# Kernel optimization log

Hardware: AMD Instinct MI355X
Metric: run time of the kernel (lower is better)

## Reference

```python
import jax, jax.numpy as jnp
import numpy as np

N_USERS = 100_000
N_ITEMS = 50_000
N_EDGES = 2_000_000
D = 64
ALPHA = 0.5      # tanh-blend coefficient (alpha)
NORM_2 = -1.0    # exponent on back-aggregation degree norm (args.norm_2)


def setup_inputs() -> dict:
    key = jax.random.key(0)
    k1, k2, k3, k4, k5 = jax.random.split(key, 5)
    return {
        "h_user": jax.random.normal(k1, (N_USERS, D), jnp.float32) * 0.1,
        "pretrained_feature": jax.random.normal(k2, (N_ITEMS, D), jnp.float32),
        "edge_w": jax.random.normal(k3, (N_ITEMS, 1), jnp.float32),
        "src_idx": jax.random.randint(k4, (N_EDGES,), 0, N_USERS, dtype=jnp.int32),
        "dst_idx": jax.random.randint(k5, (N_EDGES,), 0, N_ITEMS, dtype=jnp.int32),
    }


def reference(h_user, pretrained_feature, edge_w, src_idx, dst_idx):
    # HGCNLayer.forward: bidirectional copy_src+sum aggregation with degree norm,
    # tanh prompt blend and node-softmax edge weighting.
    ones = jnp.ones((N_EDGES,), h_user.dtype)

    # forward pass user -> item: rst[d] = sum_{(s,d) in E} h_user[s]
    rst = jax.ops.segment_sum(h_user[src_idx], dst_idx, num_segments=N_ITEMS)  # [N_ITEMS, D]
    deg_dst = jnp.clip(jax.ops.segment_sum(ones, dst_idx, num_segments=N_ITEMS), 1.0)

    # alpha * tanh prompt blend
    rst = rst + ALPHA * jnp.tanh(pretrained_feature)
    # edge-prompt softmax scaling (softmax over nodes; see notes)
    rst = jax.nn.softmax(edge_w, axis=0) * rst
    # in-degree^-1 normalization
    rst = rst / deg_dst[:, None]

    # backward pass item -> user: bsrc[s] = sum_{(s,d) in E} rst[d]
    bsrc = jax.ops.segment_sum(rst[dst_idx], src_idx, num_segments=N_USERS)  # [N_USERS, D]
    deg_src = jnp.clip(jax.ops.segment_sum(ones, src_idx, num_segments=N_USERS), 1.0)
    bsrc = bsrc * jnp.power(deg_src, NORM_2)[:, None]
    return bsrc
```

## Files before the change

### kernel.cpp

```cpp
#include <hip/hip_runtime.h>
#include <hip/hip_bf16.h>
#include <math.h>

#define N_USERS 100000
#define N_ITEMS 50000
#define N_EDGES 2000000
#define D 64

#define FB_BINS 98
#define BB_BINS 196
#define NBINS   (FB_BINS + BB_BINS)
#define CHUNK   2048
#define NCHUNK  ((N_EDGES + CHUNK - 1) / CHUNK)
#define NSH     4
#define FOFF_F_N (FB_BINS * 512 * NSH + 1)
#define FOFF_B_N (BB_BINS * 512 + 1)
#define TOTSLOT  (2 * N_EDGES)
#define PART_SLOTS (FB_BINS * 512 * NSH)
#define PASSA_WGS (((N_ITEMS + 31) / 32) * 8)
#define PASSB_WGS ((N_ITEMS + 7) / 8)
#define BWD_WGS ((N_USERS + 31) / 32)

__device__ __forceinline__ float blo(unsigned u) {
    union { unsigned i; float f; } c; c.i = u << 16; return c.f;
}
__device__ __forceinline__ float bhi(unsigned u) {
    union { unsigned i; float f; } c; c.i = u & 0xFFFF0000u; return c.f;
}
__device__ __forceinline__ unsigned bpack(float x, float y) {
    __hip_bfloat16 a = __float2bfloat16(x), b = __float2bfloat16(y);
    unsigned short ua = *reinterpret_cast<unsigned short*>(&a);
    unsigned short ub = *reinterpret_cast<unsigned short*>(&b);
    return (unsigned)ua | ((unsigned)ub << 16);
}

__global__ __launch_bounds__(256) void h2b_kernel(
    const float2* __restrict__ in, unsigned* __restrict__ out, int n) {
    int stride = gridDim.x * blockDim.x;
    for (int i = blockIdx.x * blockDim.x + threadIdx.x; i < n; i += stride) {
        float2 v = in[i];
        out[i] = bpack(v.x, v.y);
    }
}

__global__ __launch_bounds__(256) void hist_kernel(
    const int* __restrict__ src, const int* __restrict__ dst, int* __restrict__ gh) {
    __shared__ int h[NBINS];
    for (int i = threadIdx.x; i < NBINS; i += 256) h[i] = 0;
    __syncthreads();
    int stride = gridDim.x * blockDim.x;
    for (int e = blockIdx.x * blockDim.x + threadIdx.x; e < N_EDGES; e += stride) {
        atomicAdd(&h[dst[e] >> 9], 1);
        atomicAdd(&h[FB_BINS + (src[e] >> 9)], 1);
    }
    __syncthreads();
    for (int i = threadIdx.x; i < NBINS; i += 256) {
        int v = h[i];
        if (v) atomicAdd(&gh[i], v);
    }
}

__global__ void scan_excl(const int* __restrict__ in, int* __restrict__ out,
                          int* __restrict__ cur, int n) {
    const int T = 1024, E = 4;
    __shared__ int wsum[16];
    __shared__ int s_carry;
    if (threadIdx.x == 0) s_carry = 0;
    __syncthreads();

    int lane = threadIdx.x & 63;
    int wid  = threadIdx.x >> 6;

    for (int base = 0; base < n; base += T * E) {
        int idx0 = base + threadIdx.x * E;
        int v[E];
        int tot = 0;
#pragma unroll
        for (int e = 0; e < E; e++) {
            int i = idx0 + e;
            v[e] = (i < n) ? in[i] : 0;
            tot += v[e];
        }
        int incl = tot;
#pragma unroll
        for (int off = 1; off < 64; off <<= 1) {
            int t = __shfl_up(incl, off);
            if (lane >= off) incl += t;
        }
        if (lane == 63) wsum[wid] = incl;
        __syncthreads();
        if (wid == 0 && lane < 16) {
            int t = wsum[lane];
            int sc = t;
#pragma unroll
            for (int off = 1; off < 16; off <<= 1) {
                int u = __shfl_up(sc, off);
                if (lane >= off) sc += u;
            }
            wsum[lane] = sc - t;
        }
        __syncthreads();
        int wave_off = wsum[wid];
        int excl = s_carry + wave_off + incl - tot;
#pragma unroll
        for (int e = 0; e < E; e++) {
            int i = idx0 + e;
            if (i < n) { out[i] = excl; cur[i] = excl; }
            excl += v[e];
        }
        __syncthreads();
        if (threadIdx.x == T - 1) s_carry += wave_off + incl;
        __syncthreads();
    }
    if (threadIdx.x == 0) out[n] = s_carry;
}

__global__ __launch_bounds__(256) void binfill_kernel(
    const int* __restrict__ src, const int* __restrict__ dst,
    int* __restrict__ gcur, unsigned* __restrict__ stage) {
    __shared__ int cnt[NBINS];
    __shared__ int gbase[NBINS];
    __shared__ int lcur[NBINS];
    int c = blockIdx.x;
    int base = c * CHUNK;
    int nEdge = N_EDGES - base; if (nEdge > CHUNK) nEdge = CHUNK;

    for (int t = threadIdx.x; t < NBINS; t += 256) { cnt[t] = 0; lcur[t] = 0; }
    __syncthreads();

    int es[8], ed[8];
#pragma unroll
    for (int j = 0; j < 8; j++) {
        int k = j * 256 + threadIdx.x;
        if (k < nEdge) {
            es[j] = src[base + k];
            ed[j] = dst[base + k];
            atomicAdd(&cnt[ed[j] >> 9], 1);
            atomicAdd(&cnt[FB_BINS + (es[j] >> 9)], 1);
        } else {
            es[j] = -1;
        }
    }
    __syncthreads();
    for (int t = threadIdx.x; t < NBINS; t += 256) {
        int cv = cnt[t];
        gbase[t] = cv ? atomicAdd(&gcur[t], cv) : 0;
    }
    __syncthreads();
#pragma unroll
    for (int j = 0; j < 8; j++) {
        if (es[j] >= 0) {
            int s = es[j], d = ed[j];
            int bf = d >> 9;
            int p = atomicAdd(&lcur[bf], 1);
            stage[gbase[bf] + p] = (unsigned)s | ((unsigned)(d & 511) << 17);
            int bb = FB_BINS + (s >> 9);
            int q = atomicAdd(&lcur[bb], 1);
            stage[gbase[bb] + q] = (unsigned)d | ((unsigned)(s & 511) << 16);
        }
    }
}

__global__ __launch_bounds__(512) void redist3_kernel(
    const unsigned* __restrict__ stage, const int* __restrict__ binoff,
    unsigned* __restrict__ stage2, int* __restrict__ foff_f, int* __restrict__ foff_b) {
    __shared__ int cnt[512 * NSH];
    __shared__ int wsum[8];
    int wg = blockIdx.x, t = threadIdx.x, lane = t & 63, wv = t >> 6;

    if (wg < FB_BINS) {
        int B = wg;
        int beg = binoff[B], end = binoff[B + 1];
        for (int j = t; j < 512 * NSH; j += 512) cnt[j] = 0;
        __syncthreads();
        for (int k = beg + t; k < end; k += 512) {
            unsigned e = stage[k];
            atomicAdd(&cnt[(((e >> 17) & 511) << 2) | (e & 3)], 1);
        }
        __syncthreads();
        int c[NSH]; int tot = 0;
#pragma unroll
        for (int j = 0; j < NSH; j++) { c[j] = cnt[(t << 2) | j]; tot += c[j]; }
        int incl = tot;
#pragma unroll
        for (int off = 1; off < 64; off <<= 1) {
            int u = __shfl_up(incl, off);
            if (lane >= off) incl += u;
        }
        if (lane == 63) wsum[wv] = incl;
        __syncthreads();
        if (t == 0) {
            int run = 0;
#pragma unroll
            for (int k2 = 0; k2 < 8; k2++) { int x = wsum[k2]; wsum[k2] = run; run += x; }
        }
        __syncthreads();
        int base = beg + wsum[wv] + incl - tot;
        int slot0 = (((B << 9) | t) << 2);
#pragma unroll
        for (int j = 0; j < NSH; j++) {
            foff_f[slot0 + j] = base;
            cnt[(t << 2) | j] = base;
            base += c[j];
        }
        if (B == FB_BINS - 1 && t == 0) foff_f[FB_BINS * 512 * NSH] = end;
        __syncthreads();
        for (int k = beg + t; k < end; k += 512) {
            unsigned e = stage[k];
            int idx = (((e >> 17) & 511) << 2) | (e & 3);
            int p = atomicAdd(&cnt[idx], 1);
            stage2[p] = e & 0x1FFFFu;
        }
    } else {
        for (int pass = 0; pass < 2; pass++) {
            int B = FB_BINS + ((wg - FB_BINS) << 1) + pass;
            int beg = binoff[B], end = binoff[B + 1];
            cnt[t] = 0;
            __syncthreads();
            for (int k = beg + t; k < end; k += 512) {
                unsigned e = stage[k];
                atomicAdd(&cnt[(e >> 16) & 511], 1);
            }
            __syncthreads();
            int v = cnt[t];
            int incl = v;
#pragma unroll
            for (int off = 1; off < 64; off <<= 1) {
                int u = __shfl_up(incl, off);
                if (lane >= off) incl += u;
            }
            if (lane == 63) wsum[wv] = incl;
            __syncthreads();
            if (t == 0) {
                int run = 0;
#pragma unroll
                for (int k2 = 0; k2 < 8; k2++) { int x = wsum[k2]; wsum[k2] = run; run += x; }
            }
            __syncthreads();
            int base = beg + wsum[wv] + incl - v;
            foff_b[((B - FB_BINS) << 9) | t] = base;
            cnt[t] = base;
            if (B == NBINS - 1 && t == 0) foff_b[BB_BINS * 512] = end;
            __syncthreads();
            for (int k = beg + t; k < end; k += 512) {
                unsigned e = stage[k];
                int p = atomicAdd(&cnt[(e >> 16) & 511], 1);
                stage2[p] = e & 0xFFFFu;
            }
            __syncthreads();
        }
    }
}

__global__ void softmax_stats_kernel(const float* __restrict__ w, float* __restrict__ stats) {
    __shared__ float red[16];
    int tid = threadIdx.x, lane = tid & 63, wid = tid >> 6;

    float m = -INFINITY;
    for (int i = tid; i < N_ITEMS; i += 1024) m = fmaxf(m, w[i]);
#pragma unroll
    for (int off = 32; off; off >>= 1) m = fmaxf(m, __shfl_xor(m, off));
    if (lane == 0) red[wid] = m;
    __syncthreads();
    if (tid == 0) {
        float t = red[0];
        for (int k = 1; k < 16; k++) t = fmaxf(t, red[k]);
        red[0] = t;
    }
    __syncthreads();
    m = red[0];
    __syncthreads();

    float s = 0.f;
    for (int i = tid; i < N_ITEMS; i += 1024) s += expf(w[i] - m);
#pragma unroll
    for (int off = 32; off; off >>= 1) s += __shfl_xor(s, off);
    if (lane == 0) red[wid] = s;
    __syncthreads();
    if (tid == 0) {
        float t = 0.f;
        for (int k = 0; k < 16; k++) t += red[k];
        stats[0] = m;
        stats[1] = t;
    }
}

__global__ __launch_bounds__(256) void passA_fwd_kernel(
    const unsigned* __restrict__ hu16, const unsigned* __restrict__ stage2,
    const int* __restrict__ foff_f, unsigned* __restrict__ part) {
    int tid = threadIdx.x, lane = tid & 63, wv = tid >> 6;
    int q = lane & 31, half = lane >> 5;
    int ib = blockIdx.x >> 3, x = blockIdx.x & 7;
    int sh = x >> 1, hb = x & 1;
    int i0 = ib * 32 + hb * 16;

    for (int il = wv; il < 16; il += 4) {
        int i = i0 + il;
        if (i >= N_ITEMS) break;
        int slot = (i << 2) | sh;
        int a = foff_f[slot], b = foff_f[slot + 1];
        float ax = 0.f, ay = 0.f;
        int k = a;
        for (; k + 8 <= b; k += 8) {
            int s0 = (int)__builtin_nontemporal_load(&stage2[k + half]);
            int s1 = (int)__builtin_nontemporal_load(&stage2[k + 2 + half]);
            int s2 = (int)__builtin_nontemporal_load(&stage2[k + 4 + half]);
            int s3 = (int)__builtin_nontemporal_load(&stage2[k + 6 + half]);
            unsigned u0 = hu16[(s0 << 5) + q];
            unsigned u1 = hu16[(s1 << 5) + q];
            unsigned u2 = hu16[(s2 << 5) + q];
            unsigned u3 = hu16[(s3 << 5) + q];
            ax += (blo(u0) + blo(u1)) + (blo(u2) + blo(u3));
            ay += (bhi(u0) + bhi(u1)) + (bhi(u2) + bhi(u3));
        }
        for (; k + 2 <= b; k += 2) {
            unsigned u = hu16[((int)__builtin_nontemporal_load(&stage2[k + half]) << 5) + q];
            ax += blo(u); ay += bhi(u);
        }
        if (k < b && half == 0) {
            unsigned u = hu16[((int)__builtin_nontemporal_load(&stage2[k]) << 5) + q];
            ax += blo(u); ay += bhi(u);
        }
        ax += __shfl_xor(ax, 32);
        ay += __shfl_xor(ay, 32);
        if (half == 0)
            __builtin_nontemporal_store(bpack(ax, ay), &part[((size_t)slot << 5) + q]);
    }
}

__global__ __launch_bounds__(256) void passB_fwd_kernel(
    const unsigned* __restrict__ part, const float* __restrict__ pf,
    const float* __restrict__ edge_w, const int* __restrict__ foff_f,
    const float* __restrict__ stats, unsigned* __restrict__ rst16) {
    int tid = threadIdx.x, lane = tid & 63, wv = tid >> 6;
    int q = lane & 31, half = lane >> 5;
    int i = blockIdx.x * 8 + wv * 2 + half;
    if (i >= N_ITEMS) return;
    float m = stats[0], ssum = stats[1];
    float ax = 0.f, ay = 0.f;
#pragma unroll
    for (int s = 0; s < NSH; s++) {
        unsigned u = __builtin_nontemporal_load(&part[(((size_t)(i << 2) | s) << 5) + q]);
        ax += blo(u); ay += bhi(u);
    }
    int dg = foff_f[(i << 2) + 4] - foff_f[i << 2];
    float deg = dg < 1 ? 1.f : (float)dg;
    float sc = expf(edge_w[i] - m) / (ssum * deg);
    const float2* PF2 = (const float2*)pf;
    float2 pv = PF2[(size_t)i * 32 + q];
    float vx = (ax + 0.5f * tanhf(pv.x)) * sc;
    float vy = (ay + 0.5f * tanhf(pv.y)) * sc;
    rst16[(size_t)i * 32 + q] = bpack(vx, vy);
}

__global__ __launch_bounds__(256) void pass2_bwd_kernel(
    const unsigned* __restrict__ rst16, const unsigned* __restrict__ stage2,
    const int* __restrict__ foff_b, float* __restrict__ out) {
    int tid = threadIdx.x, lane = tid & 63, wv = tid >> 6;
    int q = lane & 31, half = lane >> 5;
    float2* OUT2 = (float2*)out;
    int u0i = blockIdx.x * 32;

    for (int il = wv; il < 32; il += 4) {
        int u = u0i + il;
        if (u >= N_USERS) break;
        int a = foff_b[u], b = foff_b[u + 1];
        float ax = 0.f, ay = 0.f;
        int k = a;
        for (; k + 8 <= b; k += 8) {
            int d0 = (int)__builtin_nontemporal_load(&stage2[k + half]);
            int d1 = (int)__builtin_nontemporal_load(&stage2[k + 2 + half]);
            int d2 = (int)__builtin_nontemporal_load(&stage2[k + 4 + half]);
            int d3 = (int)__builtin_nontemporal_load(&stage2[k + 6 + half]);
            unsigned u0 = rst16[(d0 << 5) + q];
            unsigned u1 = rst16[(d1 << 5) + q];
            unsigned u2 = rst16[(d2 << 5) + q];
            unsigned u3 = rst16[(d3 << 5) + q];
            ax += (blo(u0) + blo(u1)) + (blo(u2) + blo(u3));
            ay += (bhi(u0) + bhi(u1)) + (bhi(u2) + bhi(u3));
        }
        for (; k + 2 <= b; k += 2) {
            unsigned e = rst16[((int)__builtin_nontemporal_load(&stage2[k + half]) << 5) + q];
            ax += blo(e); ay += bhi(e);
        }
        if (k < b && half == 0) {
            unsigned e = rst16[((int)__builtin_nontemporal_load(&stage2[k]) << 5) + q];
            ax += blo(e); ay += bhi(e);
        }
        ax += __shfl_xor(ax, 32);
        ay += __shfl_xor(ay, 32);
        if (half == 0) {
            float deg = (float)(b - a);
            if (deg < 1.f) deg = 1.f;
            OUT2[(size_t)u * 32 + q] = make_float2(ax / deg, ay / deg);
        }
    }
}

extern "C" void kernel_launch(void* const* d_in, const int* in_sizes, int n_in,
                              void* d_out, int out_size, void* d_ws, size_t ws_size,
                              hipStream_t stream) {
    const float* h_user = (const float*)d_in[0];
    const float* pf     = (const float*)d_in[1];
    const float* edge_w = (const float*)d_in[2];
    const int*   src    = (const int*)d_in[3];
    const int*   dst    = (const int*)d_in[4];
    float* out = (float*)d_out;

    char* p = (char*)d_ws;
    int* gh      = (int*)p;     p += sizeof(int) * NBINS;
    int* binoff  = (int*)p;     p += sizeof(int) * (NBINS + 1);
    int* gcur    = (int*)p;     p += sizeof(int) * NBINS;
    int* foff_f  = (int*)p;     p += sizeof(int) * FOFF_F_N;
    int* foff_b  = (int*)p;     p += sizeof(int) * FOFF_B_N;
    float* stats = (float*)p;   p += 4 * sizeof(float);
    unsigned* part  = (unsigned*)p;
    unsigned* stage = part;
    p += sizeof(unsigned) * (size_t)PART_SLOTS * 32;
    unsigned* stage2 = (unsigned*)p; p += sizeof(unsigned) * (size_t)TOTSLOT;
    unsigned* hu16   = (unsigned*)p; p += sizeof(unsigned) * (size_t)N_USERS * 32;
    unsigned* rst16  = (unsigned*)p; p += sizeof(unsigned) * (size_t)N_ITEMS * 32;

    hipMemsetAsync(gh, 0, sizeof(int) * NBINS, stream);

    hist_kernel<<<256, 256, 0, stream>>>(src, dst, gh);
    scan_excl<<<1, 1024, 0, stream>>>(gh, binoff, gcur, NBINS);
    binfill_kernel<<<NCHUNK, 256, 0, stream>>>(src, dst, gcur, stage);
    redist3_kernel<<<196, 512, 0, stream>>>(stage, binoff, stage2, foff_f, foff_b);
    h2b_kernel<<<1024, 256, 0, stream>>>((const float2*)h_user, hu16, N_USERS * 32);
    softmax_stats_kernel<<<1, 1024, 0, stream>>>(edge_w, stats);
    passA_fwd_kernel<<<PASSA_WGS, 256, 0, stream>>>(hu16, stage2, foff_f, part);
    passB_fwd_kernel<<<PASSB_WGS, 256, 0, stream>>>(part, pf, edge_w, foff_f, stats, rst16);
    pass2_bwd_kernel<<<BWD_WGS, 256, 0, stream>>>(rst16, stage2, foff_b, out);
}
```

Measured before the change: 398.1 us.

## Fuse forward aggregation passes and merge prep kernels to cut launches

Drops the 4-way sharded forward partial-sum scheme (passA plus passB reduction through a part buffer) and replaces it with a single gather kernel per item that also applies the tanh blend, softmax scale and degree norm. The bf16 conversion of h_user is merged into the histogram kernel, and the softmax stats are merged into the scan kernel as a second block. The gather loops are unrolled to 16 edges and work-groups shrink to 16 nodes. This removes launches and the part-buffer round trip, but loses the parallelism the sharding gave to high-degree items.

Result: faster. 344.3 us (-13.5%).

```diff
diff --git a/kernel.cpp b/kernel.cpp
--- a/kernel.cpp
+++ b/kernel.cpp
@@ -12,14 +12,11 @@
 #define NBINS   (FB_BINS + BB_BINS)
 #define CHUNK   2048
 #define NCHUNK  ((N_EDGES + CHUNK - 1) / CHUNK)
-#define NSH     4
-#define FOFF_F_N (FB_BINS * 512 * NSH + 1)
+#define FOFF_F_N (FB_BINS * 512 + 1)
 #define FOFF_B_N (BB_BINS * 512 + 1)
 #define TOTSLOT  (2 * N_EDGES)
-#define PART_SLOTS (FB_BINS * 512 * NSH)
-#define PASSA_WGS (((N_ITEMS + 31) / 32) * 8)
-#define PASSB_WGS ((N_ITEMS + 7) / 8)
-#define BWD_WGS ((N_USERS + 31) / 32)
+#define FWD_WGS (N_ITEMS / 16)
+#define BWD_WGS ((N_USERS + 15) / 16)
 
 __device__ __forceinline__ float blo(unsigned u) {
     union { unsigned i; float f; } c; c.i = u << 16; return c.f;
@@ -34,22 +31,20 @@
     return (unsigned)ua | ((unsigned)ub << 16);
 }
 
-__global__ __launch_bounds__(256) void h2b_kernel(
-    const float2* __restrict__ in, unsigned* __restrict__ out, int n) {
-    int stride = gridDim.x * blockDim.x;
-    for (int i = blockIdx.x * blockDim.x + threadIdx.x; i < n; i += stride) {
-        float2 v = in[i];
-        out[i] = bpack(v.x, v.y);
-    }
-}
-
-__global__ __launch_bounds__(256) void hist_kernel(
-    const int* __restrict__ src, const int* __restrict__ dst, int* __restrict__ gh) {
+__global__ __launch_bounds__(256) void prep_kernel(
+    const float2* __restrict__ hin, unsigned* __restrict__ hu16,
+    const int* __restrict__ src, const int* __restrict__ dst,
+    int* __restrict__ gh) {
     __shared__ int h[NBINS];
     for (int i = threadIdx.x; i < NBINS; i += 256) h[i] = 0;
     __syncthreads();
     int stride = gridDim.x * blockDim.x;
-    for (int e = blockIdx.x * blockDim.x + threadIdx.x; e < N_EDGES; e += stride) {
+    int t0 = blockIdx.x * blockDim.x + threadIdx.x;
+    for (int i = t0; i < N_USERS * 32; i += stride) {
+        float2 v = hin[i];
+        hu16[i] = bpack(v.x, v.y);
+    }
+    for (int e = t0; e < N_EDGES; e += stride) {
         atomicAdd(&h[dst[e] >> 9], 1);
         atomicAdd(&h[FB_BINS + (src[e] >> 9)], 1);
     }
@@ -60,25 +55,20 @@
     }
 }
 
-__global__ void scan_excl(const int* __restrict__ in, int* __restrict__ out,
-                          int* __restrict__ cur, int n) {
-    const int T = 1024, E = 4;
+__global__ void scan_soft_kernel(const int* __restrict__ in, int* __restrict__ out,
+                                 int* __restrict__ cur,
+                                 const float* __restrict__ w, float* __restrict__ stats) {
+    __shared__ float redf[16];
     __shared__ int wsum[16];
-    __shared__ int s_carry;
-    if (threadIdx.x == 0) s_carry = 0;
-    __syncthreads();
-
-    int lane = threadIdx.x & 63;
-    int wid  = threadIdx.x >> 6;
-
-    for (int base = 0; base < n; base += T * E) {
-        int idx0 = base + threadIdx.x * E;
-        int v[E];
-        int tot = 0;
-#pragma unroll
-        for (int e = 0; e < E; e++) {
+    int tid = threadIdx.x, lane = tid & 63, wid = tid >> 6;
+
+    if (blockIdx.x == 0) {
+        int idx0 = tid * 4;
+        int v[4]; int tot = 0;
+#pragma unroll
+        for (int e = 0; e < 4; e++) {
             int i = idx0 + e;
-            v[e] = (i < n) ? in[i] : 0;
+            v[e] = (i < NBINS) ? in[i] : 0;
             tot += v[e];
         }
         int incl = tot;
@@ -100,19 +90,45 @@
             wsum[lane] = sc - t;
         }
         __syncthreads();
-        int wave_off = wsum[wid];
-        int excl = s_carry + wave_off + incl - tot;
-#pragma unroll
-        for (int e = 0; e < E; e++) {
+        int excl = wsum[wid] + incl - tot;
+#pragma unroll
+        for (int e = 0; e < 4; e++) {
             int i = idx0 + e;
-            if (i < n) { out[i] = excl; cur[i] = excl; }
+            if (i < NBINS) { out[i] = excl; cur[i] = excl; }
+            if (i == NBINS) out[i] = excl;
             excl += v[e];
         }
-        __syncthreads();
-        if (threadIdx.x == T - 1) s_carry += wave_off + incl;
-        __syncthreads();
-    }
-    if (threadIdx.x == 0) out[n] = s_carry;
+        if (tid == 1023) out[NBINS] = excl;
+        return;
+    }
+
+    float m = -INFINITY;
+    for (int i = tid; i < N_ITEMS; i += 1024) m = fmaxf(m, w[i]);
+#pragma unroll
+    for (int off = 32; off; off >>= 1) m = fmaxf(m, __shfl_xor(m, off));
+    if (lane == 0) redf[wid] = m;
+    __syncthreads();
+    if (tid == 0) {
+        float t = redf[0];
+        for (int k = 1; k < 16; k++) t = fmaxf(t, redf[k]);
+        redf[0] = t;
+    }
+    __syncthreads();
+    m = redf[0];
+    __syncthreads();
+
+    float s = 0.f;
+    for (int i = tid; i < N_ITEMS; i += 1024) s += expf(w[i] - m);
+#pragma unroll
+    for (int off = 32; off; off >>= 1) s += __shfl_xor(s, off);
+    if (lane == 0) redf[wid] = s;
+    __syncthreads();
+    if (tid == 0) {
+        float t = 0.f;
+        for (int k = 0; k < 16; k++) t += redf[k];
+        stats[0] = m;
+        stats[1] = t;
+    }
 }
 
 __global__ __launch_bounds__(256) void binfill_kernel(
@@ -164,24 +180,22 @@
 __global__ __launch_bounds__(512) void redist3_kernel(
     const unsigned* __restrict__ stage, const int* __restrict__ binoff,
     unsigned* __restrict__ stage2, int* __restrict__ foff_f, int* __restrict__ foff_b) {
-    __shared__ int cnt[512 * NSH];
+    __shared__ int cnt[512];
     __shared__ int wsum[8];
     int wg = blockIdx.x, t = threadIdx.x, lane = t & 63, wv = t >> 6;
 
     if (wg < FB_BINS) {
         int B = wg;
         int beg = binoff[B], end = binoff[B + 1];
-        for (int j = t; j < 512 * NSH; j += 512) cnt[j] = 0;
+        cnt[t] = 0;
         __syncthreads();
         for (int k = beg + t; k < end; k += 512) {
             unsigned e = stage[k];
-            atomicAdd(&cnt[(((e >> 17) & 511) << 2) | (e & 3)], 1);
-        }
-        __syncthreads();
-        int c[NSH]; int tot = 0;
-#pragma unroll
-        for (int j = 0; j < NSH; j++) { c[j] = cnt[(t << 2) | j]; tot += c[j]; }
-        int incl = tot;
+            atomicAdd(&cnt[(e >> 17) & 511], 1);
+        }
+        __syncthreads();
+        int v = cnt[t];
+        int incl = v;
 #pragma unroll
         for (int off = 1; off < 64; off <<= 1) {
             int u = __shfl_up(incl, off);
@@ -195,20 +209,14 @@
             for (int k2 = 0; k2 < 8; k2++) { int x = wsum[k2]; wsum[k2] = run; run += x; }
         }
         __syncthreads();
-        int base = beg + wsum[wv] + incl - tot;
-        int slot0 = (((B << 9) | t) << 2);
-#pragma unroll
-        for (int j = 0; j < NSH; j++) {
-            foff_f[slot0 + j] = base;
-            cnt[(t << 2) | j] = base;
-            base += c[j];
-        }
-        if (B == FB_BINS - 1 && t == 0) foff_f[FB_BINS * 512 * NSH] = end;
+        int base = beg + wsum[wv] + incl - v;
+        foff_f[(B << 9) | t] = base;
+        cnt[t] = base;
+        if (B == FB_BINS - 1 && t == 0) foff_f[FB_BINS * 512] = end;
         __syncthreads();
         for (int k = beg + t; k < end; k += 512) {
             unsigned e = stage[k];
-            int idx = (((e >> 17) & 511) << 2) | (e & 3);
-            int p = atomicAdd(&cnt[idx], 1);
+            int p = atomicAdd(&cnt[(e >> 17) & 511], 1);
             stage2[p] = e & 0x1FFFFu;
         }
     } else {
@@ -252,56 +260,46 @@
     }
 }
 
-__global__ void softmax_stats_kernel(const float* __restrict__ w, float* __restrict__ stats) {
-    __shared__ float red[16];
-    int tid = threadIdx.x, lane = tid & 63, wid = tid >> 6;
-
-    float m = -INFINITY;
-    for (int i = tid; i < N_ITEMS; i += 1024) m = fmaxf(m, w[i]);
-#pragma unroll
-    for (int off = 32; off; off >>= 1) m = fmaxf(m, __shfl_xor(m, off));
-    if (lane == 0) red[wid] = m;
-    __syncthreads();
-    if (tid == 0) {
-        float t = red[0];
-        for (int k = 1; k < 16; k++) t = fmaxf(t, red[k]);
-        red[0] = t;
-    }
-    __syncthreads();
-    m = red[0];
-    __syncthreads();
-
-    float s = 0.f;
-    for (int i = tid; i < N_ITEMS; i += 1024) s += expf(w[i] - m);
-#pragma unroll
-    for (int off = 32; off; off >>= 1) s += __shfl_xor(s, off);
-    if (lane == 0) red[wid] = s;
-    __syncthreads();
-    if (tid == 0) {
-        float t = 0.f;
-        for (int k = 0; k < 16; k++) t += red[k];
-        stats[0] = m;
-        stats[1] = t;
-    }
-}
-
-__global__ __launch_bounds__(256) void passA_fwd_kernel(
-    const unsigned* __restrict__ hu16, const unsigned* __restrict__ stage2,
-    const int* __restrict__ foff_f, unsigned* __restrict__ part) {
+__global__ __launch_bounds__(256) void fwd_gather_kernel(
+    const unsigned* __restrict__ hu16, const float* __restrict__ pf,
+    const float* __restrict__ edge_w, const unsigned* __restrict__ stage2,
+    const int* __restrict__ foff_f, const float* __restrict__ stats,
+    unsigned* __restrict__ rst16) {
     int tid = threadIdx.x, lane = tid & 63, wv = tid >> 6;
     int q = lane & 31, half = lane >> 5;
-    int ib = blockIdx.x >> 3, x = blockIdx.x & 7;
-    int sh = x >> 1, hb = x & 1;
-    int i0 = ib * 32 + hb * 16;
+    float m = stats[0], ssum = stats[1];
+    const float2* PF2 = (const float2*)pf;
+    int i0 = blockIdx.x * 16;
 
     for (int il = wv; il < 16; il += 4) {
         int i = i0 + il;
         if (i >= N_ITEMS) break;
-        int slot = (i << 2) | sh;
-        int a = foff_f[slot], b = foff_f[slot + 1];
+        int a = foff_f[i], b = foff_f[i + 1];
         float ax = 0.f, ay = 0.f;
         int k = a;
-        for (; k + 8 <= b; k += 8) {
+        for (; k + 16 <= b; k += 16) {
+            int s0 = (int)__builtin_nontemporal_load(&stage2[k + half]);
+            int s1 = (int)__builtin_nontemporal_load(&stage2[k + 2 + half]);
+            int s2 = (int)__builtin_nontemporal_load(&stage2[k + 4 + half]);
+            int s3 = (int)__builtin_nontemporal_load(&stage2[k + 6 + half]);
+            int s4 = (int)__builtin_nontemporal_load(&stage2[k + 8 + half]);
+            int s5 = (int)__builtin_nontemporal_load(&stage2[k + 10 + half]);
+            int s6 = (int)__builtin_nontemporal_load(&stage2[k + 12 + half]);
+            int s7 = (int)__builtin_nontemporal_load(&stage2[k + 14 + half]);
+            unsigned u0 = hu16[(s0 << 5) + q];
+            unsigned u1 = hu16[(s1 << 5) + q];
+            unsigned u2 = hu16[(s2 << 5) + q];
+            unsigned u3 = hu16[(s3 << 5) + q];
+            unsigned u4 = hu16[(s4 << 5) + q];
+            unsigned u5 = hu16[(s5 << 5) + q];
+            unsigned u6 = hu16[(s6 << 5) + q];
+            unsigned u7 = hu16[(s7 << 5) + q];
+            ax += ((blo(u0) + blo(u1)) + (blo(u2) + blo(u3)))
+                + ((blo(u4) + blo(u5)) + (blo(u6) + blo(u7)));
+            ay += ((bhi(u0) + bhi(u1)) + (bhi(u2) + bhi(u3)))
+                + ((bhi(u4) + bhi(u5)) + (bhi(u6) + bhi(u7)));
+        }
+        if (k + 8 <= b) {
             int s0 = (int)__builtin_nontemporal_load(&stage2[k + half]);
             int s1 = (int)__builtin_nontemporal_load(&stage2[k + 2 + half]);
             int s2 = (int)__builtin_nontemporal_load(&stage2[k + 4 + half]);
@@ -312,6 +310,7 @@
             unsigned u3 = hu16[(s3 << 5) + q];
             ax += (blo(u0) + blo(u1)) + (blo(u2) + blo(u3));
             ay += (bhi(u0) + bhi(u1)) + (bhi(u2) + bhi(u3));
+            k += 8;
         }
         for (; k + 2 <= b; k += 2) {
             unsigned u = hu16[((int)__builtin_nontemporal_load(&stage2[k + half]) << 5) + q];
@@ -323,51 +322,55 @@
         }
         ax += __shfl_xor(ax, 32);
         ay += __shfl_xor(ay, 32);
-        if (half == 0)
-            __builtin_nontemporal_store(bpack(ax, ay), &part[((size_t)slot << 5) + q]);
-    }
-}
-
-__global__ __launch_bounds__(256) void passB_fwd_kernel(
-    const unsigned* __restrict__ part, const float* __restrict__ pf,
-    const float* __restrict__ edge_w, const int* __restrict__ foff_f,
-    const float* __restrict__ stats, unsigned* __restrict__ rst16) {
-    int tid = threadIdx.x, lane = tid & 63, wv = tid >> 6;
-    int q = lane & 31, half = lane >> 5;
-    int i = blockIdx.x * 8 + wv * 2 + half;
-    if (i >= N_ITEMS) return;
-    float m = stats[0], ssum = stats[1];
-    float ax = 0.f, ay = 0.f;
-#pragma unroll
-    for (int s = 0; s < NSH; s++) {
-        unsigned u = __builtin_nontemporal_load(&part[(((size_t)(i << 2) | s) << 5) + q]);
-        ax += blo(u); ay += bhi(u);
-    }
-    int dg = foff_f[(i << 2) + 4] - foff_f[i << 2];
-    float deg = dg < 1 ? 1.f : (float)dg;
-    float sc = expf(edge_w[i] - m) / (ssum * deg);
-    const float2* PF2 = (const float2*)pf;
-    float2 pv = PF2[(size_t)i * 32 + q];
-    float vx = (ax + 0.5f * tanhf(pv.x)) * sc;
-    float vy = (ay + 0.5f * tanhf(pv.y)) * sc;
-    rst16[(size_t)i * 32 + q] = bpack(vx, vy);
-}
-
-__global__ __launch_bounds__(256) void pass2_bwd_kernel(
+        if (half == 0) {
+            float deg = (float)(b - a);
+            if (deg < 1.f) deg = 1.f;
+            float sc = expf(edge_w[i] - m) / (ssum * deg);
+            float2 pv = PF2[(size_t)i * 32 + q];
+            float vx = (ax + 0.5f * tanhf(pv.x)) * sc;
+            float vy = (ay + 0.5f * tanhf(pv.y)) * sc;
+            rst16[(size_t)i * 32 + q] = bpack(vx, vy);
+        }
+    }
+}
+
+__global__ __launch_bounds__(256) void bwd_gather_kernel(
     const unsigned* __restrict__ rst16, const unsigned* __restrict__ stage2,
     const int* __restrict__ foff_b, float* __restrict__ out) {
     int tid = threadIdx.x, lane = tid & 63, wv = tid >> 6;
     int q = lane & 31, half = lane >> 5;
     float2* OUT2 = (float2*)out;
-    int u0i = blockIdx.x * 32;
-
-    for (int il = wv; il < 32; il += 4) {
+    int u0i = blockIdx.x * 16;
+
+    for (int il = wv; il < 16; il += 4) {
         int u = u0i + il;
         if (u >= N_USERS) break;
         int a = foff_b[u], b = foff_b[u + 1];
         float ax = 0.f, ay = 0.f;
         int k = a;
-        for (; k + 8 <= b; k += 8) {
+        for (; k + 16 <= b; k += 16) {
+            int d0 = (int)__builtin_nontemporal_load(&stage2[k + half]);
+            int d1 = (int)__builtin_nontemporal_load(&stage2[k + 2 + half]);
+            int d2 = (int)__builtin_nontemporal_load(&stage2[k + 4 + half]);
+            int d3 = (int)__builtin_nontemporal_load(&stage2[k + 6 + half]);
+            int d4 = (int)__builtin_nontemporal_load(&stage2[k + 8 + half]);
+            int d5 = (int)__builtin_nontemporal_load(&stage2[k + 10 + half]);
+            int d6 = (int)__builtin_nontemporal_load(&stage2[k + 12 + half]);
+            int d7 = (int)__builtin_nontemporal_load(&stage2[k + 14 + half]);
+            unsigned u0 = rst16[(d0 << 5) + q];
+            unsigned u1 = rst16[(d1 << 5) + q];
+            unsigned u2 = rst16[(d2 << 5) + q];
+            unsigned u3 = rst16[(d3 << 5) + q];
+            unsigned u4 = rst16[(d4 << 5) + q];
+            unsigned u5 = rst16[(d5 << 5) + q];
+            unsigned u6 = rst16[(d6 << 5) + q];
+            unsigned u7 = rst16[(d7 << 5) + q];
+            ax += ((blo(u0) + blo(u1)) + (blo(u2) + blo(u3)))
+                + ((blo(u4) + blo(u5)) + (blo(u6) + blo(u7)));
+            ay += ((bhi(u0) + bhi(u1)) + (bhi(u2) + bhi(u3)))
+                + ((bhi(u4) + bhi(u5)) + (bhi(u6) + bhi(u7)));
+        }
+        if (k + 8 <= b) {
             int d0 = (int)__builtin_nontemporal_load(&stage2[k + half]);
             int d1 = (int)__builtin_nontemporal_load(&stage2[k + 2 + half]);
             int d2 = (int)__builtin_nontemporal_load(&stage2[k + 4 + half]);
@@ -378,6 +381,7 @@
             unsigned u3 = rst16[(d3 << 5) + q];
             ax += (blo(u0) + blo(u1)) + (blo(u2) + blo(u3));
             ay += (bhi(u0) + bhi(u1)) + (bhi(u2) + bhi(u3));
+            k += 8;
         }
         for (; k + 2 <= b; k += 2) {
             unsigned e = rst16[((int)__builtin_nontemporal_load(&stage2[k + half]) << 5) + q];
@@ -414,22 +418,17 @@
     int* foff_f  = (int*)p;     p += sizeof(int) * FOFF_F_N;
     int* foff_b  = (int*)p;     p += sizeof(int) * FOFF_B_N;
     float* stats = (float*)p;   p += 4 * sizeof(float);
-    unsigned* part  = (unsigned*)p;
-    unsigned* stage = part;
-    p += sizeof(unsigned) * (size_t)PART_SLOTS * 32;
+    unsigned* stage  = (unsigned*)p; p += sizeof(unsigned) * (size_t)TOTSLOT;
     unsigned* stage2 = (unsigned*)p; p += sizeof(unsigned) * (size_t)TOTSLOT;
     unsigned* hu16   = (unsigned*)p; p += sizeof(unsigned) * (size_t)N_USERS * 32;
     unsigned* rst16  = (unsigned*)p; p += sizeof(unsigned) * (size_t)N_ITEMS * 32;
 
     hipMemsetAsync(gh, 0, sizeof(int) * NBINS, stream);
 
-    hist_kernel<<<256, 256, 0, stream>>>(src, dst, gh);
-    scan_excl<<<1, 1024, 0, stream>>>(gh, binoff, gcur, NBINS);
+    prep_kernel<<<1024, 256, 0, stream>>>((const float2*)h_user, hu16, src, dst, gh);
+    scan_soft_kernel<<<2, 1024, 0, stream>>>(gh, binoff, gcur, edge_w, stats);
     binfill_kernel<<<NCHUNK, 256, 0, stream>>>(src, dst, gcur, stage);
     redist3_kernel<<<196, 512, 0, stream>>>(stage, binoff, stage2, foff_f, foff_b);
-    h2b_kernel<<<1024, 256, 0, stream>>>((const float2*)h_user, hu16, N_USERS * 32);
-    softmax_stats_kernel<<<1, 1024, 0, stream>>>(edge_w, stats);
-    passA_fwd_kernel<<<PASSA_WGS, 256, 0, stream>>>(hu16, stage2, foff_f, part);
-    passB_fwd_kernel<<<PASSB_WGS, 256, 0, stream>>>(part, pf, edge_w, foff_f, stats, rst16);
-    pass2_bwd_kernel<<<BWD_WGS, 256, 0, stream>>>(rst16, stage2, foff_b, out);
-}
+    fwd_gather_kernel<<<FWD_WGS, 256, 0, stream>>>(hu16, pf, edge_w, stage2, foff_f, stats, rst16);
+    bwd_gather_kernel<<<BWD_WGS, 256, 0, stream>>>(rst16, stage2, foff_b, out);
+}
```
